# Performance work log

Hardware: AMD Instinct MI355X
Metric: run time of the kernel (lower is better)

## Reference

```python
import jax, jax.numpy as jnp
import numpy as np

B, S, D, H = 2, 2048, 1024, 16
DEPTH = D // H


def setup_inputs() -> dict:
    key = jax.random.key(0)
    ks = jax.random.split(key, 10)
    std = 1.0 / np.sqrt(D)
    v = jax.random.normal(ks[0], (B, S, D), jnp.float32)
    q = jax.random.normal(ks[1], (B, S, D), jnp.float32)
    k = jax.random.normal(ks[2], (B, S, D), jnp.float32)
    # padding mask: 1.0 at masked (padded) key positions, 0.0 elsewhere
    mask = (jax.random.uniform(ks[3], (B, 1, 1, S)) < 0.1).astype(jnp.float32)
    Wq = jax.random.normal(ks[4], (D, D), jnp.float32) * std
    bq = jnp.zeros((D,), jnp.float32)
    Wv = jax.random.normal(ks[5], (D, D), jnp.float32) * std
    bv = jnp.zeros((D,), jnp.float32)
    Wo = jax.random.normal(ks[6], (D, D), jnp.float32) * std
    bo = jnp.zeros((D,), jnp.float32)
    return {"v": v, "q": q, "k": k, "mask": mask,
            "Wq": Wq, "bq": bq, "Wv": Wv, "bv": bv, "Wo": Wo, "bo": bo}


def _split_heads(x):
    # (B, S, D) -> (B, H, S, depth)
    return x.reshape(B, S, H, DEPTH).transpose(0, 2, 1, 3)


def reference(v, q, k, mask, Wq, bq, Wv, bv, Wo, bo):
    # NOTE: faithful to source, keys are projected with the QUERY weights
    # (mixedK = self.wQuery(k) in the original code).
    Q = _split_heads(q @ Wq + bq)
    K = _split_heads(k @ Wq + bq)
    V = _split_heads(v @ Wv + bv)
    scale = 1.0 / jnp.sqrt(jnp.asarray(DEPTH, jnp.float32))
    logits = jnp.einsum('bhqd,bhkd->bhqk', Q, K) * scale
    logits = logits + mask * (-1e9)
    attn = jax.nn.softmax(logits, axis=-1)
    out = jnp.einsum('bhqk,bhkd->bhqd', attn, V)
    out = out.transpose(0, 2, 1, 3).reshape(B, S, D)
    return out @ Wo + bo
```

## Files before the change

kernel.cpp:

```cpp
#include <hip/hip_runtime.h>
#include <cstddef>


namespace {

constexpr int Ss = 2048;
constexpr int Dd = 1024;
constexpr int Mm = 4096;
constexpr float QSCALE = 0.18033688f;
constexpr float NEG2 = -1.442695041e9f;

typedef unsigned short u16;
typedef __attribute__((ext_vector_type(8))) __bf16 bf16x8;
typedef __attribute__((ext_vector_type(4))) float f32x4;
typedef __attribute__((ext_vector_type(16))) float f32x16;
typedef __attribute__((ext_vector_type(4))) unsigned int u32x4;
typedef __attribute__((ext_vector_type(2))) unsigned int u32x2;
typedef __attribute__((ext_vector_type(8))) unsigned short us8;

__device__ __forceinline__ u16 bfc(float f) {
  __bf16 h = (__bf16)f;
  return __builtin_bit_cast(u16, h);
}
__device__ __forceinline__ unsigned pack2(float lo, float hi) {
  return (unsigned)bfc(lo) | ((unsigned)bfc(hi) << 16);
}

__device__ __forceinline__ void gload_lds16(const void* g, void* l) {
  __builtin_amdgcn_global_load_lds(
      (__attribute__((address_space(1))) void*)g,
      (__attribute__((address_space(3))) void*)l, 16, 0, 0);
}

__device__ __forceinline__ f32x4 mfma16(bf16x8 a, bf16x8 b, f32x4 c) {
  return __builtin_amdgcn_mfma_f32_16x16x32_bf16(a, b, c, 0, 0, 0);
}
__device__ __forceinline__ f32x16 mfma32(bf16x8 a, bf16x8 b, f32x16 c) {
  return __builtin_amdgcn_mfma_f32_32x32x16_bf16(a, b, c, 0, 0, 0);
}
__device__ __forceinline__ float exp2_fast(float x) {
  return __builtin_amdgcn_exp2f(x);
}

__device__ __forceinline__ void pl32swap(unsigned& a, unsigned& b) {
#if __has_builtin(__builtin_amdgcn_permlane32_swap)
  u32x2 r = __builtin_amdgcn_permlane32_swap(a, b, false, false);
  a = r[0];
  b = r[1];
#else
  unsigned ax = (unsigned)__shfl_xor((int)a, 32);
  unsigned bx = (unsigned)__shfl_xor((int)b, 32);
  bool hi = (threadIdx.x & 63) >= 32;
  unsigned na = hi ? bx : a;
  unsigned nb = hi ? b : ax;
  a = na;
  b = nb;
#endif
}

#define PIPE_BARRIER_V(N)                                  \
  do {                                                     \
    asm volatile("s_waitcnt vmcnt(" #N ")" ::: "memory");  \
    __builtin_amdgcn_sched_barrier(0);                     \
    __builtin_amdgcn_s_barrier();                          \
    __builtin_amdgcn_sched_barrier(0);                     \
  } while (0)

__device__ __forceinline__ int swz(int row, int col) {
  return row * 64 + ((((col >> 3) ^ (row & 7)) << 3) | (col & 7));
}
__device__ __forceinline__ int src_col(int lane) {
  return ((lane & 7) ^ (lane >> 3)) * 8;
}

__global__ __launch_bounds__(256) void prep(const float* __restrict__ W0,
                                            const float* __restrict__ W1,
                                            const float* __restrict__ W2,
                                            const float* __restrict__ q,
                                            const float* __restrict__ k,
                                            const float* __restrict__ v,
                                            u16* __restrict__ wsbase,
                                            u16* __restrict__ qb,
                                            u16* __restrict__ kb,
                                            u16* __restrict__ vb) {
  __shared__ float tile[32][33];
  const int blk = (int)blockIdx.x;
  const int tid = threadIdx.x;
  if (blk < 3072) {
    const int z = blk >> 10;
    const int rem = blk & 1023;
    const int n0 = (rem & 31) * 32;
    const int k0 = (rem >> 5) * 32;
    const float* W = (z == 0) ? W0 : (z == 1) ? W1 : W2;
    u16* WT = wsbase + (size_t)z * (1024 * 1024);
    const int tx = tid & 31;
    const int ty = tid >> 5;
#pragma unroll
    for (int i = 0; i < 4; ++i)
      tile[ty + i * 8][tx] = W[(size_t)(k0 + ty + i * 8) * 1024 + n0 + tx];
    __syncthreads();
    const int r = tid >> 3;
    const int c4 = (tid & 7) * 4;
    ushort4 o4 = make_ushort4(bfc(tile[c4 + 0][r]), bfc(tile[c4 + 1][r]),
                              bfc(tile[c4 + 2][r]), bfc(tile[c4 + 3][r]));
    *(ushort4*)(&WT[(size_t)(n0 + r) * 1024 + k0 + c4]) = o4;
  } else {
    const int e = blk - 3072;
    const int which = e >> 11;
    const int b2 = e & 2047;
    const float* src = (which == 0) ? q : (which == 1) ? k : v;
    u16* dst = (which == 0) ? qb : (which == 1) ? kb : vb;
    const int base = (b2 * 256 + tid) * 8;
    const float4 a = *(const float4*)(src + base);
    const float4 b = *(const float4*)(src + base + 4);
    us8 o;
    o[0] = bfc(a.x); o[1] = bfc(a.y); o[2] = bfc(a.z); o[3] = bfc(a.w);
    o[4] = bfc(b.x); o[5] = bfc(b.y); o[6] = bfc(b.z); o[7] = bfc(b.w);
    *(us8*)(dst + base) = o;
  }
}

__global__ __launch_bounds__(256) void proj_qkv(
    const u16* __restrict__ qb, const u16* __restrict__ kb,
    const u16* __restrict__ vb, const u16* __restrict__ WqT,
    const u16* __restrict__ WvT, const float* __restrict__ bq,
    const float* __restrict__ bv, const float* __restrict__ maskf,
    u16* __restrict__ Qp, u16* __restrict__ Kp, u16* __restrict__ VpT) {
  constexpr int K = 1024, N = 1024, M = 4096;
  __shared__ u16 As[128 * 64];
  __shared__ u16 Bs[64 * 64];
  const int lin = (int)blockIdx.x;
  const int xcd = lin & 7;
  const int j = lin >> 3;
  const int panel = xcd * 12 + (j >> 4);
  const int ntile = j & 15;
  const int z = panel >> 5;
  const int mtile = panel & 31;
  const int n0 = ntile * 64;
  const int m0 = mtile * 128;

  const u16* A = (z == 0) ? qb : (z == 1) ? kb : vb;
  const u16* Bt = (z == 2) ? WvT : WqT;
  const float* bias = (z == 2) ? bv : bq;
  const float cscale = (z == 0) ? QSCALE : 1.0f;

  const int tid = threadIdx.x;
  const int wid = tid >> 6;
  const int lane = tid & 63;
  const int g = lane >> 4;
  const int lr = lane & 15;

  const f32x4 zero = {0.f, 0.f, 0.f, 0.f};
  f32x4 acc[2][4];
#pragma unroll
  for (int m = 0; m < 2; ++m)
#pragma unroll
    for (int n = 0; n < 4; ++n) acc[m][n] = zero;

  for (int kt = 0; kt < 16; ++kt) {
#pragma unroll
    for (int jj = 0; jj < 4; ++jj) {
      int rb = (wid * 4 + jj) * 8;
      gload_lds16(&A[(size_t)(m0 + rb + (lane >> 3)) * K + kt * 64 + src_col(lane)],
                  &As[rb * 64]);
    }
#pragma unroll
    for (int jj = 0; jj < 2; ++jj) {
      int rb = (wid * 2 + jj) * 8;
      gload_lds16(&Bt[(size_t)(n0 + rb + (lane >> 3)) * K + kt * 64 + src_col(lane)],
                  &Bs[rb * 64]);
    }
    __syncthreads();
#pragma unroll
    for (int kk = 0; kk < 2; ++kk) {
      bf16x8 a[2], b[4];
#pragma unroll
      for (int m = 0; m < 2; ++m)
        a[m] = *(const bf16x8*)(&As[swz(wid * 32 + m * 16 + lr, kk * 32 + g * 8)]);
#pragma unroll
      for (int n = 0; n < 4; ++n)
        b[n] = *(const bf16x8*)(&Bs[swz(n * 16 + lr, kk * 32 + g * 8)]);
#pragma unroll
      for (int m = 0; m < 2; ++m)
#pragma unroll
        for (int n = 0; n < 4; ++n) acc[m][n] = mfma16(a[m], b[n], acc[m][n]);
    }
    __syncthreads();
  }

#pragma unroll
  for (int n = 0; n < 4; ++n) {
    const int col = n0 + n * 16 + lr;
    const float bv_ = bias[col];
#pragma unroll
    for (int m = 0; m < 2; ++m) {
      const int rowb = m0 + wid * 32 + m * 16 + g * 4;
      if (z == 2) {
        const f32x4 mk = *(const f32x4*)(&maskf[rowb]);
        ushort4 o4;
        o4.x = (mk[0] != 0.f) ? (u16)0 : bfc(acc[m][n][0] + bv_);
        o4.y = (mk[1] != 0.f) ? (u16)0 : bfc(acc[m][n][1] + bv_);
        o4.z = (mk[2] != 0.f) ? (u16)0 : bfc(acc[m][n][2] + bv_);
        o4.w = (mk[3] != 0.f) ? (u16)0 : bfc(acc[m][n][3] + bv_);
        *(ushort4*)(&VpT[(size_t)col * M + rowb]) = o4;
      } else {
        u16* Cp = (z == 0) ? Qp : Kp;
#pragma unroll
        for (int r = 0; r < 4; ++r)
          Cp[(size_t)(rowb + r) * N + col] = bfc((acc[m][n][r] + bv_) * cscale);
      }
    }
  }
}

__global__ __launch_bounds__(256) void gemm_o(const u16* __restrict__ Ap,
                                              const u16* __restrict__ Bt,
                                              const float* __restrict__ bias,
                                              float* __restrict__ Cp) {
  constexpr int K = 1024, N = 1024;
  __shared__ u16 As[64 * 64];
  __shared__ u16 Bs[64 * 64];
  const int lin = (int)blockIdx.x;
  const int xcd = lin & 7;
  const int j = lin >> 3;
  const int mtile = xcd * 8 + (j >> 4);
  const int ntile = j & 15;
  const int n0 = ntile * 64;
  const int m0 = mtile * 64;

  const int tid = threadIdx.x;
  const int wid = tid >> 6;
  const int lane = tid & 63;
  const int l31 = lane & 31;
  const int hi = lane >> 5;
  const int wr = wid >> 1, wc = wid & 1;

  f32x16 acc;
#pragma unroll
  for (int r = 0; r < 16; ++r) acc[r] = 0.f;

  for (int kt = 0; kt < 16; ++kt) {
#pragma unroll
    for (int jj = 0; jj < 2; ++jj) {
      const int rb = (wid * 2 + jj) * 8;
      gload_lds16(&Ap[(size_t)(m0 + rb + (lane >> 3)) * K + kt * 64 + src_col(lane)],
                  &As[rb * 64]);
      gload_lds16(&Bt[(size_t)(n0 + rb + (lane >> 3)) * K + kt * 64 + src_col(lane)],
                  &Bs[rb * 64]);
    }
    __syncthreads();
#pragma unroll
    for (int d = 0; d < 4; ++d) {
      bf16x8 af = *(const bf16x8*)(&As[swz(wr * 32 + l31, d * 16 + hi * 8)]);
      bf16x8 bf = *(const bf16x8*)(&Bs[swz(wc * 32 + l31, d * 16 + hi * 8)]);
      acc = mfma32(af, bf, acc);
    }
    __syncthreads();
  }
  const int col = n0 + wc * 32 + l31;
  const float bv_ = bias[col];
#pragma unroll
  for (int r = 0; r < 16; ++r) {
    const int row = m0 + wr * 32 + (r & 3) + 8 * (r >> 2) + 4 * hi;
    Cp[(size_t)row * N + col] = acc[r] + bv_;
  }
}

__global__ __launch_bounds__(512) void attn32(const u16* __restrict__ Qp,
                                              const u16* __restrict__ Kp,
                                              const u16* __restrict__ VpT,
                                              const float* __restrict__ mask,
                                              u16* __restrict__ Op) {
  __shared__ u16 smem[8 * 64 * 64];
  __shared__ float msall[Ss];
  const int tid = threadIdx.x;
  const int wid = tid >> 6;
  const int lane = tid & 63;
  const int l31 = lane & 31;
  const int hi = lane >> 5;
  const int qq = wid & 3;
  const int kh = wid >> 2;
  const int lin = (int)(blockIdx.x + (blockIdx.y << 4));
  const int wl = (lin & 7) * 64 + (lin >> 3);
  const int qt = wl & 15;
  const int bh = wl >> 4;
  const int b = bh >> 4;
  const int h = bh & 15;
  const int q0 = qt * 128;
  const size_t base = ((size_t)b * Ss) * Dd + (size_t)h * 64;
  const size_t vbase = (size_t)h * 64 * Mm + (size_t)b * Ss;
  const int qrow = q0 + qq * 32 + l31;

  auto stageKV = [&](int t, int buf) {
    const int key0 = t * 64;
    const int rb = wid * 8;
    gload_lds16(&Kp[base + (size_t)(key0 + rb + (lane >> 3)) * Dd + src_col(lane)],
                smem + buf * 4096 + rb * 64);
    gload_lds16(&VpT[vbase + (size_t)(rb + (lane >> 3)) * Mm + key0 + src_col(lane)],
                smem + (4 + buf) * 4096 + rb * 64);
  };

  const float4 mk = *(const float4*)(&mask[(size_t)b * Ss + tid * 4]);
  bf16x8 qf[4];
#pragma unroll
  for (int d = 0; d < 4; ++d)
    qf[d] = *(const bf16x8*)(&Qp[base + (size_t)qrow * Dd + d * 16 + hi * 8]);

  stageKV(0, 0);
  stageKV(1, 1);

  {
    f32x4 s = {mk.x * NEG2, mk.y * NEG2, mk.z * NEG2, mk.w * NEG2};
    *(f32x4*)(&msall[tid * 4]) = s;
  }
  asm volatile("s_waitcnt lgkmcnt(0)" ::: "memory");
  __builtin_amdgcn_sched_barrier(0);
  __builtin_amdgcn_s_barrier();
  __builtin_amdgcn_sched_barrier(0);

  f32x16 oacc[2];
#pragma unroll
  for (int i = 0; i < 2; ++i)
#pragma unroll
    for (int r = 0; r < 16; ++r) oacc[i][r] = 0.f;
  float lsum = 0.f;

  for (int i = 0; i < 16; ++i) {
    PIPE_BARRIER_V(0);
    if (i < 15) {
      stageKV(2 * i + 2, (2 * i + 2) & 3);
      stageKV(2 * i + 3, (2 * i + 3) & 3);
    }
#pragma unroll
    for (int u = 0; u < 2; ++u) {
      const int t = 2 * i + u;
      const int buf = t & 3;
      const u16* ks = smem + buf * 4096;
      const u16* vt = smem + (4 + buf) * 4096;
      const float* msp = &msall[t * 64 + kh * 32];

      f32x16 sacc;
#pragma unroll
      for (int a = 0; a < 4; ++a) {
        const f32x4 mv = *(const f32x4*)(&msp[a * 8 + hi * 4]);
#pragma unroll
        for (int jj = 0; jj < 4; ++jj) sacc[a * 4 + jj] = mv[jj];
      }
      __builtin_amdgcn_s_setprio(1);
#pragma unroll
      for (int d = 0; d < 4; ++d) {
        bf16x8 kf = *(const bf16x8*)(&ks[swz(kh * 32 + l31, d * 16 + hi * 8)]);
        sacc = mfma32(kf, qf[d], sacc);
      }
      __builtin_amdgcn_s_setprio(0);

#pragma unroll
      for (int r = 0; r < 16; ++r) sacc[r] = exp2_fast(sacc[r]);

      {
        float sm[8];
#pragma unroll
        for (int r = 0; r < 8; ++r) sm[r] = sacc[r] + sacc[r + 8];
#pragma unroll
        for (int s = 4; s >= 1; s >>= 1)
#pragma unroll
          for (int r = 0; r < s; ++r) sm[r] += sm[r + s];
        lsum += sm[0] + __shfl_xor(sm[0], 32);
      }

      bf16x8 pa[2];
#pragma unroll
      for (int slot = 0; slot < 2; ++slot) {
        const int bse = slot * 8;
        unsigned A0 = pack2(sacc[bse + 0], sacc[bse + 1]);
        unsigned A1 = pack2(sacc[bse + 2], sacc[bse + 3]);
        unsigned B0 = pack2(sacc[bse + 4], sacc[bse + 5]);
        unsigned B1 = pack2(sacc[bse + 6], sacc[bse + 7]);
        pl32swap(A0, B0);
        pl32swap(A1, B1);
        u32x4 w = {A0, A1, B0, B1};
        pa[slot] = __builtin_bit_cast(bf16x8, w);
      }

      __builtin_amdgcn_s_setprio(1);
#pragma unroll
      for (int slot = 0; slot < 2; ++slot)
#pragma unroll
        for (int dsub = 0; dsub < 2; ++dsub) {
          bf16x8 vf = *(const bf16x8*)(
              &vt[swz(dsub * 32 + l31, kh * 32 + slot * 16 + hi * 8)]);
          oacc[dsub] = mfma32(pa[slot], vf, oacc[dsub]);
        }
      __builtin_amdgcn_s_setprio(0);
    }
  }

  __syncthreads();
  float* rbuf = (float*)smem;
  if (kh == 1) {
    float* p = rbuf + qq * 3072 + lane;
#pragma unroll
    for (int r = 0; r < 16; ++r) p[r * 64] = oacc[0][r];
#pragma unroll
    for (int r = 0; r < 16; ++r) p[(16 + r) * 64] = oacc[1][r];
    if (hi == 0) rbuf[12288 + qq * 32 + l31] = lsum;
  }
  __syncthreads();
  if (kh == 0) {
    const float* p = rbuf + qq * 3072 + lane;
#pragma unroll
    for (int r = 0; r < 16; ++r) oacc[0][r] += p[r * 64];
#pragma unroll
    for (int r = 0; r < 16; ++r) oacc[1][r] += p[(16 + r) * 64];
    const float ltot = lsum + rbuf[12288 + qq * 32 + l31];
    float* lrow = rbuf + 12800 + qq * 32;
    if (hi == 0) lrow[l31] = __builtin_amdgcn_rcpf(ltot);
    f32x4 rl[4];
#pragma unroll
    for (int a = 0; a < 4; ++a)
      rl[a] = *(const f32x4*)(&lrow[a * 8 + hi * 4]);
#pragma unroll
    for (int dsub = 0; dsub < 2; ++dsub) {
      const int col = h * 64 + dsub * 32 + l31;
#pragma unroll
      for (int r = 0; r < 16; ++r) {
        const int row = q0 + qq * 32 + (r & 3) + 8 * (r >> 2) + 4 * hi;
        Op[((size_t)b * Ss + row) * Dd + col] =
            bfc(oacc[dsub][r] * rl[r >> 2][r & 3]);
      }
    }
  }
}

}

extern "C" void kernel_launch(void* const* d_in, const int* in_sizes, int n_in,
                              void* d_out, int out_size, void* d_ws, size_t ws_size,
                              hipStream_t stream) {
  (void)in_sizes; (void)n_in; (void)out_size; (void)ws_size;
  const float* v = (const float*)d_in[0];
  const float* q = (const float*)d_in[1];
  const float* k = (const float*)d_in[2];
  const float* mask = (const float*)d_in[3];
  const float* Wq = (const float*)d_in[4];
  const float* bq = (const float*)d_in[5];
  const float* Wv = (const float*)d_in[6];
  const float* bv = (const float*)d_in[7];
  const float* Wo = (const float*)d_in[8];
  const float* bo = (const float*)d_in[9];
  float* out = (float*)d_out;

  constexpr size_t MEG = 1024 * 1024;
  u16* ws = (u16*)d_ws;
  u16* WqT = ws;
  u16* WvT = ws + 1 * MEG;
  u16* WoT = ws + 2 * MEG;
  u16* qb  = ws + 3 * MEG;
  u16* kb  = ws + 7 * MEG;
  u16* vb  = ws + 11 * MEG;
  u16* Qp  = ws + 15 * MEG;
  u16* Kp  = ws + 19 * MEG;
  u16* VpT = ws + 23 * MEG;
  u16* AO  = qb;

  prep<<<dim3(3072 + 6144), 256, 0, stream>>>(Wq, Wv, Wo, q, k, v, ws, qb, kb, vb);
  proj_qkv<<<dim3(1536), 256, 0, stream>>>(qb, kb, vb, WqT, WvT, bq, bv, mask,
                                           Qp, Kp, VpT);
  attn32<<<dim3(16, 32), 512, 0, stream>>>(Qp, Kp, VpT, mask, AO);
  gemm_o<<<dim3(1024), 256, 0, stream>>>(AO, WoT, bo, out);
}
```

Measured before the change: 119.8 us.

## Fuse fp32-to-bf16 activation conversion into QKV projection GEMM loads

Drops the separate pass in prep that converts q/k/v from fp32 to bf16 in workspace. The projection GEMM now reads fp32 activations directly into registers, converts them to bf16 and writes them into swizzled LDS. This removes a full extra read and write of the activations plus part of a launch. In exchange each GEMM tile reads twice the bytes for A, and the async LDS load is replaced by a synchronous register-staged load, which may expose latency. Activation rows are reread by every N-tile, so the fp32 traffic is multiplied.

```diff
diff --git a/kernel.cpp b/kernel.cpp
--- a/kernel.cpp
+++ b/kernel.cpp
@@ -76,53 +76,32 @@
 __global__ __launch_bounds__(256) void prep(const float* __restrict__ W0,
                                             const float* __restrict__ W1,
                                             const float* __restrict__ W2,
-                                            const float* __restrict__ q,
-                                            const float* __restrict__ k,
-                                            const float* __restrict__ v,
-                                            u16* __restrict__ wsbase,
-                                            u16* __restrict__ qb,
-                                            u16* __restrict__ kb,
-                                            u16* __restrict__ vb) {
+                                            u16* __restrict__ wsbase) {
   __shared__ float tile[32][33];
   const int blk = (int)blockIdx.x;
   const int tid = threadIdx.x;
-  if (blk < 3072) {
-    const int z = blk >> 10;
-    const int rem = blk & 1023;
-    const int n0 = (rem & 31) * 32;
-    const int k0 = (rem >> 5) * 32;
-    const float* W = (z == 0) ? W0 : (z == 1) ? W1 : W2;
-    u16* WT = wsbase + (size_t)z * (1024 * 1024);
-    const int tx = tid & 31;
-    const int ty = tid >> 5;
-#pragma unroll
-    for (int i = 0; i < 4; ++i)
-      tile[ty + i * 8][tx] = W[(size_t)(k0 + ty + i * 8) * 1024 + n0 + tx];
-    __syncthreads();
-    const int r = tid >> 3;
-    const int c4 = (tid & 7) * 4;
-    ushort4 o4 = make_ushort4(bfc(tile[c4 + 0][r]), bfc(tile[c4 + 1][r]),
-                              bfc(tile[c4 + 2][r]), bfc(tile[c4 + 3][r]));
-    *(ushort4*)(&WT[(size_t)(n0 + r) * 1024 + k0 + c4]) = o4;
-  } else {
-    const int e = blk - 3072;
-    const int which = e >> 11;
-    const int b2 = e & 2047;
-    const float* src = (which == 0) ? q : (which == 1) ? k : v;
-    u16* dst = (which == 0) ? qb : (which == 1) ? kb : vb;
-    const int base = (b2 * 256 + tid) * 8;
-    const float4 a = *(const float4*)(src + base);
-    const float4 b = *(const float4*)(src + base + 4);
-    us8 o;
-    o[0] = bfc(a.x); o[1] = bfc(a.y); o[2] = bfc(a.z); o[3] = bfc(a.w);
-    o[4] = bfc(b.x); o[5] = bfc(b.y); o[6] = bfc(b.z); o[7] = bfc(b.w);
-    *(us8*)(dst + base) = o;
-  }
+  const int z = blk >> 10;
+  const int rem = blk & 1023;
+  const int n0 = (rem & 31) * 32;
+  const int k0 = (rem >> 5) * 32;
+  const float* W = (z == 0) ? W0 : (z == 1) ? W1 : W2;
+  u16* WT = wsbase + (size_t)z * (1024 * 1024);
+  const int tx = tid & 31;
+  const int ty = tid >> 5;
+#pragma unroll
+  for (int i = 0; i < 4; ++i)
+    tile[ty + i * 8][tx] = W[(size_t)(k0 + ty + i * 8) * 1024 + n0 + tx];
+  __syncthreads();
+  const int r = tid >> 3;
+  const int c4 = (tid & 7) * 4;
+  ushort4 o4 = make_ushort4(bfc(tile[c4 + 0][r]), bfc(tile[c4 + 1][r]),
+                            bfc(tile[c4 + 2][r]), bfc(tile[c4 + 3][r]));
+  *(ushort4*)(&WT[(size_t)(n0 + r) * 1024 + k0 + c4]) = o4;
 }
 
 __global__ __launch_bounds__(256) void proj_qkv(
-    const u16* __restrict__ qb, const u16* __restrict__ kb,
-    const u16* __restrict__ vb, const u16* __restrict__ WqT,
+    const float* __restrict__ qf32, const float* __restrict__ kf32,
+    const float* __restrict__ vf32, const u16* __restrict__ WqT,
     const u16* __restrict__ WvT, const float* __restrict__ bq,
     const float* __restrict__ bv, const float* __restrict__ maskf,
     u16* __restrict__ Qp, u16* __restrict__ Kp, u16* __restrict__ VpT) {
@@ -139,7 +118,7 @@
   const int n0 = ntile * 64;
   const int m0 = mtile * 128;
 
-  const u16* A = (z == 0) ? qb : (z == 1) ? kb : vb;
+  const float* A = (z == 0) ? qf32 : (z == 1) ? kf32 : vf32;
   const u16* Bt = (z == 2) ? WvT : WqT;
   const float* bias = (z == 2) ? bv : bq;
   const float cscale = (z == 0) ? QSCALE : 1.0f;
@@ -149,6 +128,8 @@
   const int lane = tid & 63;
   const int g = lane >> 4;
   const int lr = lane & 15;
+  const int arow = tid >> 1;
+  const int ac4 = (tid & 1) * 32;
 
   const f32x4 zero = {0.f, 0.f, 0.f, 0.f};
   f32x4 acc[2][4];
@@ -158,17 +139,21 @@
     for (int n = 0; n < 4; ++n) acc[m][n] = zero;
 
   for (int kt = 0; kt < 16; ++kt) {
-#pragma unroll
-    for (int jj = 0; jj < 4; ++jj) {
-      int rb = (wid * 4 + jj) * 8;
-      gload_lds16(&A[(size_t)(m0 + rb + (lane >> 3)) * K + kt * 64 + src_col(lane)],
-                  &As[rb * 64]);
-    }
+    float4 areg[8];
+#pragma unroll
+    for (int i = 0; i < 8; ++i)
+      areg[i] = *(const float4*)(&A[(size_t)(m0 + arow) * K + kt * 64 + ac4 + i * 4]);
 #pragma unroll
     for (int jj = 0; jj < 2; ++jj) {
       int rb = (wid * 2 + jj) * 8;
       gload_lds16(&Bt[(size_t)(n0 + rb + (lane >> 3)) * K + kt * 64 + src_col(lane)],
                   &Bs[rb * 64]);
+    }
+#pragma unroll
+    for (int i = 0; i < 8; ++i) {
+      ushort4 o4 = make_ushort4(bfc(areg[i].x), bfc(areg[i].y),
+                                bfc(areg[i].z), bfc(areg[i].w));
+      *(ushort4*)(&As[swz(arow, ac4 + i * 4)]) = o4;
     }
     __syncthreads();
 #pragma unroll
@@ -455,16 +440,13 @@
   u16* WqT = ws;
   u16* WvT = ws + 1 * MEG;
   u16* WoT = ws + 2 * MEG;
-  u16* qb  = ws + 3 * MEG;
-  u16* kb  = ws + 7 * MEG;
-  u16* vb  = ws + 11 * MEG;
+  u16* AO  = ws + 3 * MEG;
   u16* Qp  = ws + 15 * MEG;
   u16* Kp  = ws + 19 * MEG;
   u16* VpT = ws + 23 * MEG;
-  u16* AO  = qb;
-
-  prep<<<dim3(3072 + 6144), 256, 0, stream>>>(Wq, Wv, Wo, q, k, v, ws, qb, kb, vb);
-  proj_qkv<<<dim3(1536), 256, 0, stream>>>(qb, kb, vb, WqT, WvT, bq, bv, mask,
+
+  prep<<<dim3(3072), 256, 0, stream>>>(Wq, Wv, Wo, ws);
+  proj_qkv<<<dim3(1536), 256, 0, stream>>>(q, k, v, WqT, WvT, bq, bv, mask,
                                            Qp, Kp, VpT);
   attn32<<<dim3(16, 32), 512, 0, stream>>>(Qp, Kp, VpT, mask, AO);
   gemm_o<<<dim3(1024), 256, 0, stream>>>(AO, WoT, bo, out);
```

Result: slower. 173.2 us (+44.5%).
